# Kernel tuning notes

Hardware: AMD Instinct MI355X
Metric: run time of the kernel (lower is better)

Reference implementation:

```python
import jax, jax.numpy as jnp
import numpy as np

B, N, D = 8, 2048, 1024

def setup_inputs() -> dict:
    key = jax.random.key(0)
    ks = jax.random.split(key, 4)
    x = jax.random.normal(ks[0], (B, N, D), dtype=jnp.float32)
    # Glorot-uniform-like scaling as keras Dense default
    def glorot(k, shape):
        fan_in, fan_out = shape[0], shape[1]
        lim = jnp.sqrt(6.0 / (fan_in + fan_out)).astype(jnp.float32)
        return jax.random.uniform(k, shape, jnp.float32, -lim, lim)
    Wq = glorot(ks[1], (D, D))
    Wk = glorot(ks[2], (D, D))
    Wout = glorot(ks[3], (N, D))  # out_proj acts on last axis of [B,N,N] scores
    bq = jnp.zeros((D,), jnp.float32)
    bk = jnp.zeros((D,), jnp.float32)
    bout = jnp.zeros((D,), jnp.float32)
    return {"x": x, "Wq": Wq, "bq": bq, "Wk": Wk, "bk": bk, "Wout": Wout, "bout": bout}

def reference(x, Wq, bq, Wk, bk, Wout, bout):
    Q = x @ Wq + bq                                  # [B,N,D]
    K = x @ Wk + bk                                  # [B,N,D]
    scores = jnp.einsum("bnd,bmd->bnm", Q, K)       # [B,N,N] (no 1/sqrt(d) in source)
    A = jax.nn.softmax(scores, axis=-1)              # [B,N,N]
    return A @ Wout + bout                           # [B,N,D]
```

## Files before the change

### kernel.cpp

```cpp
#include <hip/hip_runtime.h>


typedef unsigned short u16;
typedef __bf16 bf16x8 __attribute__((ext_vector_type(8)));
typedef float f32x4 __attribute__((ext_vector_type(4)));

#define BB 8
#define NN 2048
#define DD 1024
#define MT (BB * NN)
#define PSTRIDE 4096

#define MFMA3(d, ah, al, bh, bl)                                         \
  d = __builtin_amdgcn_mfma_f32_16x16x32_bf16(ah, bh, d, 0, 0, 0);       \
  d = __builtin_amdgcn_mfma_f32_16x16x32_bf16(ah, bl, d, 0, 0, 0);       \
  d = __builtin_amdgcn_mfma_f32_16x16x32_bf16(al, bh, d, 0, 0, 0);

static __device__ __forceinline__ u16 f2bf(float f) {
  unsigned u = __builtin_bit_cast(unsigned, f);
  u += 0x7FFFu + ((u >> 16) & 1u);
  return (u16)(u >> 16);
}
static __device__ __forceinline__ float bf2f(u16 h) {
  unsigned u = ((unsigned)h) << 16;
  return __builtin_bit_cast(float, u);
}

static __device__ __forceinline__ void gload16(const void* g, void* l) {
  __builtin_amdgcn_global_load_lds((const __attribute__((address_space(1))) void*)g,
                                   (__attribute__((address_space(3))) void*)l, 16, 0, 0);
}

static __device__ __forceinline__ int swz_wg() {
  int nwg = gridDim.x;
  int orig = blockIdx.x;
  int q = nwg >> 3;
  return (orig & 7) * q + (orig >> 3);
}

#define SW(r) (((r) ^ ((r) >> 2)) & 3)

static __device__ __forceinline__ void stage_plane_sw(const u16* __restrict__ g0,
                                                      u16* lp0, int tid) {
#pragma unroll
  for (int j = 0; j < 2; j++) {
    int o = tid + j * 512;
    int row = o >> 2, c = o & 3;
    const u16* g = g0 + (size_t)row * DD + ((c ^ SW(row)) << 3);
    u16* lp = lp0 + (((tid >> 6) << 6) + j * 512) * 8;
    gload16(g, lp);
  }
}

static __device__ __forceinline__ bf16x8 rdfrag(const u16* plane, int row, int g4) {
  return *(const bf16x8*)&plane[row * 32 + ((g4 ^ SW(row)) << 3)];
}

template <bool STG, int VM>
static __device__ __forceinline__ void tile4(
    u16* Lc, const u16* Ah, const u16* Al, const u16* Bh, const u16* Bl, int kst,
    f32x4 (&acc)[8][4], int tid, int wm, int wn, int r16, int g4) {
  u16* PA0 = Lc;
  u16* PA1 = Lc + 8192;
  u16* PB0 = Lc + 16384;
  u16* PB1 = Lc + 24576;
  bf16x8 a0[4], a1[4], b0[4], b1[4];

#pragma unroll
  for (int fm = 0; fm < 4; fm++) {
    int rw = wm * 128 + fm * 16 + r16;
    a0[fm] = rdfrag(PA0, rw, g4);
    a1[fm] = rdfrag(PA1, rw, g4);
  }
#pragma unroll
  for (int fn = 0; fn < 2; fn++) {
    int rw = wn * 64 + fn * 16 + r16;
    b0[fn] = rdfrag(PB0, rw, g4);
    b1[fn] = rdfrag(PB1, rw, g4);
  }
  __builtin_amdgcn_s_barrier();
  asm volatile("s_waitcnt lgkmcnt(0)" ::: "memory");
  __builtin_amdgcn_s_setprio(1);
#pragma unroll
  for (int fm = 0; fm < 4; fm++)
#pragma unroll
    for (int fn = 0; fn < 2; fn++) { MFMA3(acc[fm][fn], a0[fm], a1[fm], b0[fn], b1[fn]); }
  __builtin_amdgcn_s_setprio(0);

#pragma unroll
  for (int fn = 2; fn < 4; fn++) {
    int rw = wn * 64 + fn * 16 + r16;
    b0[fn] = rdfrag(PB0, rw, g4);
    b1[fn] = rdfrag(PB1, rw, g4);
  }
  __builtin_amdgcn_s_barrier();
  asm volatile("s_waitcnt lgkmcnt(0)" ::: "memory");
  __builtin_amdgcn_s_setprio(1);
#pragma unroll
  for (int fm = 0; fm < 4; fm++)
#pragma unroll
    for (int fn = 2; fn < 4; fn++) { MFMA3(acc[fm][fn], a0[fm], a1[fm], b0[fn], b1[fn]); }
  __builtin_amdgcn_s_setprio(0);
  __builtin_amdgcn_s_barrier();

#pragma unroll
  for (int fm = 0; fm < 4; fm++) {
    int rw = wm * 128 + 64 + fm * 16 + r16;
    a0[fm] = rdfrag(PA0, rw, g4);
    a1[fm] = rdfrag(PA1, rw, g4);
  }
  if (STG) {
    stage_plane_sw(Bh + kst, PB0, tid);
    stage_plane_sw(Bl + kst, PB1, tid);
  }
  __builtin_amdgcn_s_barrier();
  asm volatile("s_waitcnt lgkmcnt(0)" ::: "memory");
  __builtin_amdgcn_s_setprio(1);
#pragma unroll
  for (int fm = 0; fm < 4; fm++)
#pragma unroll
    for (int fn = 0; fn < 2; fn++) { MFMA3(acc[fm + 4][fn], a0[fm], a1[fm], b0[fn], b1[fn]); }
  __builtin_amdgcn_s_setprio(0);
  __builtin_amdgcn_s_barrier();

  if (STG) {
    stage_plane_sw(Ah + kst, PA0, tid);
    stage_plane_sw(Al + kst, PA1, tid);
  }
  if (VM == 8) {
    asm volatile("s_waitcnt vmcnt(8)" ::: "memory");
  } else if (VM == 0) {
    asm volatile("s_waitcnt vmcnt(0)" ::: "memory");
  }
  __builtin_amdgcn_s_barrier();
  __builtin_amdgcn_s_setprio(1);
#pragma unroll
  for (int fm = 0; fm < 4; fm++)
#pragma unroll
    for (int fn = 2; fn < 4; fn++) { MFMA3(acc[fm + 4][fn], a0[fm], a1[fm], b0[fn], b1[fn]); }
  __builtin_amdgcn_s_setprio(0);
}

static __device__ __forceinline__ void mm8_core(u16* L, const u16* Ah, const u16* Al,
                                                const u16* Bh, const u16* Bl,
                                                f32x4 (&acc)[8][4], int tid) {
  int lane = tid & 63, r16 = lane & 15, g4 = lane >> 4;
  int w = tid >> 6, wm = w >> 2, wn = w & 3;
  u16* L0 = L;
  u16* L1 = L + 4 * 8192;
  stage_plane_sw(Ah + 0, L0 + 0, tid);
  stage_plane_sw(Al + 0, L0 + 8192, tid);
  stage_plane_sw(Bh + 0, L0 + 16384, tid);
  stage_plane_sw(Bl + 0, L0 + 24576, tid);
  stage_plane_sw(Ah + 32, L1 + 0, tid);
  stage_plane_sw(Al + 32, L1 + 8192, tid);
  stage_plane_sw(Bh + 32, L1 + 16384, tid);
  stage_plane_sw(Bl + 32, L1 + 24576, tid);
  asm volatile("s_waitcnt vmcnt(8)" ::: "memory");
  __builtin_amdgcn_s_barrier();
#pragma unroll 1
  for (int i = 0; i < 15; i++) {
    int t0 = 2 * i;
    tile4<true, 8>(L0, Ah, Al, Bh, Bl, (t0 + 2) * 32, acc, tid, wm, wn, r16, g4);
    tile4<true, 8>(L1, Ah, Al, Bh, Bl, (t0 + 3) * 32, acc, tid, wm, wn, r16, g4);
  }
  tile4<false, 0>(L0, Ah, Al, Bh, Bl, 0, acc, tid, wm, wn, r16, g4);
  tile4<false, -1>(L1, Ah, Al, Bh, Bl, 0, acc, tid, wm, wn, r16, g4);
}

__launch_bounds__(512, 2)
__global__ void k_gemm_s8(const u16* __restrict__ yh, const u16* __restrict__ yl,
                          const u16* __restrict__ xh, const u16* __restrict__ xl,
                          float* __restrict__ S) {
  __shared__ __attribute__((aligned(16))) u16 lds[2][4][8192];
  int wg = swz_wg();
  int nt = wg & 7, mtot = wg >> 3;
  int b = mtot >> 3, mt = mtot & 7;
  const size_t po = (size_t)b * NN * DD;
  const u16* Ah = yh + po + (size_t)(mt * 256) * DD;
  const u16* Al = yl + po + (size_t)(mt * 256) * DD;
  const u16* Bh = xh + po + (size_t)(nt * 256) * DD;
  const u16* Bl = xl + po + (size_t)(nt * 256) * DD;
  int tid = threadIdx.x;
  f32x4 acc[8][4] = {};
  mm8_core(&lds[0][0][0], Ah, Al, Bh, Bl, acc, tid);
  int lane = tid & 63, r16 = lane & 15, g4 = lane >> 4;
  int w = tid >> 6, wm = w >> 2, wn = w & 3;
  float* Sb = S + (size_t)b * NN * NN;
#pragma unroll
  for (int fm = 0; fm < 8; fm++)
#pragma unroll
    for (int fn = 0; fn < 4; fn++) {
      int col = nt * 256 + wn * 64 + fn * 16 + r16;
      int row = mt * 256 + wm * 128 + fm * 16 + g4 * 4;
#pragma unroll
      for (int i2 = 0; i2 < 4; i2++)
        Sb[(size_t)(row + i2) * NN + col] = acc[fm][fn][i2];
    }
}

__launch_bounds__(512, 2)
__global__ void k_gemm_y8(const u16* __restrict__ ah_g, const u16* __restrict__ al_g,
                          const u16* __restrict__ bh_g, const u16* __restrict__ bl_g,
                          u16* __restrict__ ohi, u16* __restrict__ olo) {
  __shared__ __attribute__((aligned(16))) u16 lds[2][4][8192];
  int wg = swz_wg();
  int nt = wg & 3, mt = wg >> 2;
  const u16* Ah = ah_g + (size_t)(mt * 256) * DD;
  const u16* Al = al_g + (size_t)(mt * 256) * DD;
  const u16* Bh = bh_g + (size_t)(nt * 256) * DD;
  const u16* Bl = bl_g + (size_t)(nt * 256) * DD;
  int tid = threadIdx.x;
  f32x4 acc[8][4] = {};
  mm8_core(&lds[0][0][0], Ah, Al, Bh, Bl, acc, tid);
  int lane = tid & 63, r16 = lane & 15, g4 = lane >> 4;
  int w = tid >> 6, wm = w >> 2, wn = w & 3;
#pragma unroll
  for (int fm = 0; fm < 8; fm++)
#pragma unroll
    for (int fn = 0; fn < 4; fn++) {
      int col = nt * 256 + wn * 64 + fn * 16 + r16;
      int row = mt * 256 + wm * 128 + fm * 16 + g4 * 4;
#pragma unroll
      for (int i2 = 0; i2 < 4; i2++) {
        float v = acc[fm][fn][i2];
        u16 h = f2bf(v);
        size_t o = (size_t)(row + i2) * DD + col;
        ohi[o] = h;
        olo[o] = f2bf(v - bf2f(h));
      }
    }
}

__global__ void k_split(const float* __restrict__ x, u16* __restrict__ hi,
                        u16* __restrict__ lo, long n4) {
  long i = (long)blockIdx.x * blockDim.x + threadIdx.x;
  long stride = (long)gridDim.x * blockDim.x;
  for (; i < n4; i += stride) {
    float4 v = ((const float4*)x)[i];
    u16 h0 = f2bf(v.x), h1 = f2bf(v.y), h2 = f2bf(v.z), h3 = f2bf(v.w);
    ushort4 hv; hv.x = h0; hv.y = h1; hv.z = h2; hv.w = h3;
    ushort4 lv;
    lv.x = f2bf(v.x - bf2f(h0)); lv.y = f2bf(v.y - bf2f(h1));
    lv.z = f2bf(v.z - bf2f(h2)); lv.w = f2bf(v.w - bf2f(h3));
    ((ushort4*)hi)[i] = hv;
    ((ushort4*)lo)[i] = lv;
  }
}

__global__ void k_transpose_split(const float* __restrict__ W, u16* __restrict__ thi,
                                  int R, int C) {
  __shared__ float tile[32][33];
  int c0 = blockIdx.x * 32, r0 = blockIdx.y * 32;
  int tx = threadIdx.x, ty = threadIdx.y;
#pragma unroll
  for (int i = 0; i < 4; i++)
    tile[ty + i * 8][tx] = W[(size_t)(r0 + ty + i * 8) * C + c0 + tx];
  __syncthreads();
#pragma unroll
  for (int i = 0; i < 4; i++) {
    float v = tile[tx][ty + i * 8];
    thi[(size_t)(c0 + ty + i * 8) * R + r0 + tx] = f2bf(v);
  }
}

__global__ void k_matvec(const float* __restrict__ A, const float* __restrict__ v,
                         float* __restrict__ out, int cols) {
  int w = threadIdx.x >> 6, lane = threadIdx.x & 63;
  int row = blockIdx.x * 4 + w;
  const float4* Ar = (const float4*)(A + (size_t)row * cols);
  const float4* vv = (const float4*)v;
  float s = 0.f;
  for (int j = lane; j < cols / 4; j += 64) {
    float4 a = Ar[j], b = vv[j];
    s += a.x * b.x + a.y * b.y + a.z * b.z + a.w * b.w;
  }
#pragma unroll
  for (int o = 32; o > 0; o >>= 1) s += __shfl_xor(s, o);
  if (lane == 0) out[row] = s;
}

__global__ void k_softmax(float* __restrict__ S, const float* __restrict__ c2, int nrows) {
  int w = threadIdx.x >> 6, lane = threadIdx.x & 63;
  int row = blockIdx.x * 4 + w;
  if (row >= nrows) return;
  const float4* Sr = (const float4*)(S + (size_t)row * NN);
  const float4* c2b = (const float4*)(c2 + ((size_t)(row >> 11) << 11));
  float4 v[8];
  float mx = -3.4e38f;
#pragma unroll
  for (int j = 0; j < 8; j++) {
    v[j] = Sr[j * 64 + lane];
    float4 c = c2b[j * 64 + lane];
    v[j].x += c.x; v[j].y += c.y; v[j].z += c.z; v[j].w += c.w;
    mx = fmaxf(mx, fmaxf(fmaxf(v[j].x, v[j].y), fmaxf(v[j].z, v[j].w)));
  }
#pragma unroll
  for (int o = 32; o > 0; o >>= 1) mx = fmaxf(mx, __shfl_xor(mx, o));
  float e[32];
  float sum = 0.f;
#pragma unroll
  for (int j = 0; j < 8; j++) {
    e[j * 4 + 0] = __expf(v[j].x - mx);
    e[j * 4 + 1] = __expf(v[j].y - mx);
    e[j * 4 + 2] = __expf(v[j].z - mx);
    e[j * 4 + 3] = __expf(v[j].w - mx);
    sum += e[j * 4 + 0] + e[j * 4 + 1] + e[j * 4 + 2] + e[j * 4 + 3];
  }
#pragma unroll
  for (int o = 32; o > 0; o >>= 1) sum += __shfl_xor(sum, o);
  float inv = 1.0f / sum;
  ushort4* Pr = (ushort4*)((u16*)S + (size_t)row * PSTRIDE);
#pragma unroll
  for (int j = 0; j < 8; j++) {
    ushort4 pv;
    pv.x = f2bf(e[j * 4 + 0] * inv);
    pv.y = f2bf(e[j * 4 + 1] * inv);
    pv.z = f2bf(e[j * 4 + 2] * inv);
    pv.w = f2bf(e[j * 4 + 3] * inv);
    Pr[j * 64 + lane] = pv;
  }
}

static __device__ __forceinline__ void stage_tile(const u16* __restrict__ gsrc,
                                                  u16* plane, int t, int ldg) {
  int w = t >> 6;
#pragma unroll
  for (int j = 0; j < 2; j++) {
    int idx = t + j * 256;
    const u16* g = gsrc + (size_t)(idx >> 2) * ldg + (idx & 3) * 8;
    u16* lp = plane + (w * 64 + j * 256) * 8;
    gload16(g, lp);
  }
}

__launch_bounds__(256)
__global__ void k_gemm_out(const u16* __restrict__ P, const u16* __restrict__ woutT,
                           const float* __restrict__ bout, float* __restrict__ out) {
  __shared__ __attribute__((aligned(16))) u16 lds[2][128][32];
  int wg = swz_wg();
  int b = wg >> 7, dt = wg & 7, ntt = (wg >> 3) & 15;
  const u16* Pb = P + (size_t)b * NN * PSTRIDE;
  float* ob = out + (size_t)b * NN * DD;

  int t = threadIdx.x, lane = t & 63, w = t >> 6;
  int wr = w >> 1, wc = w & 1, r16 = lane & 15, g = lane >> 4;

  f32x4 acc[4][4] = {};

  for (int k0 = 0; k0 < NN; k0 += 32) {
    stage_tile(Pb + (size_t)(ntt * 128) * PSTRIDE + k0, &lds[0][0][0], t, PSTRIDE);
    stage_tile(woutT + (size_t)(dt * 128) * NN + k0, &lds[1][0][0], t, NN);
    __syncthreads();
    bf16x8 bh[4];
#pragma unroll
    for (int fn = 0; fn < 4; fn++)
      bh[fn] = *(const bf16x8*)&lds[1][wc * 64 + fn * 16 + r16][g * 8];
#pragma unroll
    for (int fm = 0; fm < 4; fm++) {
      bf16x8 ah = *(const bf16x8*)&lds[0][wr * 64 + fm * 16 + r16][g * 8];
#pragma unroll
      for (int fn = 0; fn < 4; fn++)
        acc[fm][fn] = __builtin_amdgcn_mfma_f32_16x16x32_bf16(ah, bh[fn], acc[fm][fn], 0, 0, 0);
    }
    __syncthreads();
  }
#pragma unroll
  for (int fm = 0; fm < 4; fm++) {
#pragma unroll
    for (int fn = 0; fn < 4; fn++) {
      int col = dt * 128 + wc * 64 + fn * 16 + r16;
      float bv = bout[col];
      int row = ntt * 128 + wr * 64 + fm * 16 + g * 4;
#pragma unroll
      for (int i = 0; i < 4; i++)
        ob[(size_t)(row + i) * DD + col] = acc[fm][fn][i] + bv;
    }
  }
}

extern "C" void kernel_launch(void* const* d_in, const int* in_sizes, int n_in,
                              void* d_out, int out_size, void* d_ws, size_t ws_size,
                              hipStream_t stream) {
  const float* x = (const float*)d_in[0];
  const float* Wq = (const float*)d_in[1];
  const float* bq = (const float*)d_in[2];
  const float* Wk = (const float*)d_in[3];
  const float* bk = (const float*)d_in[4];
  const float* Wout = (const float*)d_in[5];
  const float* bout = (const float*)d_in[6];
  float* out = (float*)d_out;
  char* ws = (char*)d_ws;

  const size_t MB = 1ull << 20;
  u16* mth = (u16*)(ws + 0 * MB);
  u16* mtl = (u16*)(ws + 2 * MB);
  u16* woutT = (u16*)(ws + 4 * MB);
  float* v2 = (float*)(ws + 8 * MB);
  float* c2 = (float*)(ws + 8 * MB + 65536);
  char* base = ws + 12 * MB;

  dim3 tb(32, 8, 1);

  if (ws_size >= 204 * MB) {
    u16* xh = (u16*)(base);
    u16* xl = (u16*)(base + 32 * MB);
    u16* yh = (u16*)(base + 64 * MB);
    u16* yl = (u16*)(base + 96 * MB);
    char* R = base + 128 * MB;
    u16* wqh = (u16*)(R);
    u16* wql = (u16*)(R + 2 * MB);
    u16* wkh = (u16*)(R + 4 * MB);
    u16* wkl = (u16*)(R + 6 * MB);
    float* S = (float*)R;

    k_split<<<256, 256, 0, stream>>>(Wq, wqh, wql, (long)DD * DD / 4);
    k_split<<<256, 256, 0, stream>>>(Wk, wkh, wkl, (long)DD * DD / 4);
    k_gemm_y8<<<16, 512, 0, stream>>>(wkh, wkl, wqh, wql, mth, mtl);
    k_transpose_split<<<dim3(32, 64, 1), tb, 0, stream>>>(Wout, woutT, 2048, 1024);
    k_matvec<<<256, 256, 0, stream>>>(Wk, bq, v2, DD);
    k_matvec<<<4096, 256, 0, stream>>>(x, v2, c2, DD);
    k_split<<<2048, 256, 0, stream>>>(x, xh, xl, (long)MT * DD / 4);
    k_gemm_y8<<<256, 512, 0, stream>>>(xh, xl, mth, mtl, yh, yl);
    for (int h = 0; h < 2; h++) {
      size_t qo = (size_t)h * 4 * NN * DD;
      k_gemm_s8<<<256, 512, 0, stream>>>(yh + qo, yl + qo, xh + qo, xl + qo, S);
      k_softmax<<<4 * NN / 4, 256, 0, stream>>>(S, c2 + (size_t)h * 4 * NN, 4 * NN);
      k_gemm_out<<<4 * 128, 256, 0, stream>>>((const u16*)S, woutT, bout, out + qo);
    }
  } else if (ws_size >= 156 * MB) {
    u16* xh = (u16*)(base);
    u16* xl = (u16*)(base + 32 * MB);
    u16* yh = (u16*)(base + 64 * MB);
    u16* yl = (u16*)(base + 96 * MB);
    char* R = base + 128 * MB;
    u16* wqh = (u16*)(R);
    u16* wql = (u16*)(R + 2 * MB);
    u16* wkh = (u16*)(R + 4 * MB);
    u16* wkl = (u16*)(R + 6 * MB);
    float* S = (float*)R;

    k_split<<<256, 256, 0, stream>>>(Wq, wqh, wql, (long)DD * DD / 4);
    k_split<<<256, 256, 0, stream>>>(Wk, wkh, wkl, (long)DD * DD / 4);
    k_gemm_y8<<<16, 512, 0, stream>>>(wkh, wkl, wqh, wql, mth, mtl);
    k_transpose_split<<<dim3(32, 64, 1), tb, 0, stream>>>(Wout, woutT, 2048, 1024);
    k_matvec<<<256, 256, 0, stream>>>(Wk, bq, v2, DD);
    k_matvec<<<4096, 256, 0, stream>>>(x, v2, c2, DD);
    k_split<<<2048, 256, 0, stream>>>(x, xh, xl, (long)MT * DD / 4);
    k_gemm_y8<<<256, 512, 0, stream>>>(xh, xl, mth, mtl, yh, yl);
    for (int b = 0; b < BB; b++) {
      size_t qo = (size_t)b * NN * DD;
      k_gemm_s8<<<64, 512, 0, stream>>>(yh + qo, yl + qo, xh + qo, xl + qo, S);
      k_softmax<<<NN / 4, 256, 0, stream>>>(S, c2 + (size_t)b * NN, NN);
      k_gemm_out<<<128, 256, 0, stream>>>((const u16*)S, woutT, bout, out + qo);
    }
  } else {
    u16* xh = (u16*)(base);
    u16* xl = (u16*)(base + 8 * MB);
    u16* yh = (u16*)(base + 16 * MB);
    u16* yl = (u16*)(base + 24 * MB);
    char* R = base + 32 * MB;
    u16* wqh = (u16*)(R);
    u16* wql = (u16*)(R + 2 * MB);
    u16* wkh = (u16*)(R + 4 * MB);
    u16* wkl = (u16*)(R + 6 * MB);
    float* S = (float*)R;

    k_split<<<256, 256, 0, stream>>>(Wq, wqh, wql, (long)DD * DD / 4);
    k_split<<<256, 256, 0, stream>>>(Wk, wkh, wkl, (long)DD * DD / 4);
    k_gemm_y8<<<16, 512, 0, stream>>>(wkh, wkl, wqh, wql, mth, mtl);
    k_transpose_split<<<dim3(32, 64, 1), tb, 0, stream>>>(Wout, woutT, 2048, 1024);
    k_matvec<<<256, 256, 0, stream>>>(Wk, bq, v2, DD);
    k_matvec<<<4096, 256, 0, stream>>>(x, v2, c2, DD);
    for (int c = 0; c < 4; c++) {
      size_t xo = (size_t)c * 2 * NN * DD;
      k_split<<<1024, 256, 0, stream>>>(x + xo, xh, xl, (long)2 * NN * DD / 4);
      k_gemm_y8<<<64, 512, 0, stream>>>(xh, xl, mth, mtl, yh, yl);
      for (int bi = 0; bi < 2; bi++) {
        size_t lo = (size_t)bi * NN * DD;
        k_gemm_s8<<<64, 512, 0, stream>>>(yh + lo, yl + lo, xh + lo, xl + lo, S);
        k_softmax<<<NN / 4, 256, 0, stream>>>(S, c2 + (size_t)(c * 2 + bi) * NN, NN);
        k_gemm_out<<<128, 256, 0, stream>>>((const u16*)S, woutT, bout, out + xo + lo);
      }
    }
  }
}
```

Measured before the change: 522.7 us.

## Load A fragments directly from global into registers, stage only B in LDS

The GEMM core stops staging the A operand (hi/lo bf16 planes) through LDS. Each wave now reads its A fragments straight from global memory into registers, while B stays double-buffered in LDS. This halves LDS usage, removes several barriers per k-step and reorders the MFMA blocks. In exchange, A reads become uncoalesced 16-byte per-lane global loads, more vector registers are held, and the vmcnt wait depths change.

```diff
diff --git a/kernel.cpp b/kernel.cpp
--- a/kernel.cpp
+++ b/kernel.cpp
@@ -58,19 +58,16 @@
 
 template <bool STG, int VM>
 static __device__ __forceinline__ void tile4(
-    u16* Lc, const u16* Ah, const u16* Al, const u16* Bh, const u16* Bl, int kst,
-    f32x4 (&acc)[8][4], int tid, int wm, int wn, int r16, int g4) {
-  u16* PA0 = Lc;
-  u16* PA1 = Lc + 8192;
-  u16* PB0 = Lc + 16384;
-  u16* PB1 = Lc + 24576;
-  bf16x8 a0[4], a1[4], b0[4], b1[4];
-
-#pragma unroll
-  for (int fm = 0; fm < 4; fm++) {
-    int rw = wm * 128 + fm * 16 + r16;
-    a0[fm] = rdfrag(PA0, rw, g4);
-    a1[fm] = rdfrag(PA1, rw, g4);
+    u16* Lc, const u16* aPH, const u16* aPL, const u16* Bh, const u16* Bl,
+    int k0, int kst, f32x4 (&acc)[8][4], int tid, int wn, int r16, int g4) {
+  u16* PB0 = Lc;
+  u16* PB1 = Lc + 8192;
+  bf16x8 aH[8], aL[8], b0[4], b1[4];
+
+#pragma unroll
+  for (int fm = 0; fm < 8; fm++) {
+    aH[fm] = *(const bf16x8*)(aPH + (size_t)fm * 16 * DD + k0);
+    aL[fm] = *(const bf16x8*)(aPL + (size_t)fm * 16 * DD + k0);
   }
 #pragma unroll
   for (int fn = 0; fn < 2; fn++) {
@@ -78,13 +75,11 @@
     b0[fn] = rdfrag(PB0, rw, g4);
     b1[fn] = rdfrag(PB1, rw, g4);
   }
-  __builtin_amdgcn_s_barrier();
-  asm volatile("s_waitcnt lgkmcnt(0)" ::: "memory");
   __builtin_amdgcn_s_setprio(1);
 #pragma unroll
   for (int fm = 0; fm < 4; fm++)
 #pragma unroll
-    for (int fn = 0; fn < 2; fn++) { MFMA3(acc[fm][fn], a0[fm], a1[fm], b0[fn], b1[fn]); }
+    for (int fn = 0; fn < 2; fn++) { MFMA3(acc[fm][fn], aH[fm], aL[fm], b0[fn], b1[fn]); }
   __builtin_amdgcn_s_setprio(0);
 
 #pragma unroll
@@ -93,51 +88,39 @@
     b0[fn] = rdfrag(PB0, rw, g4);
     b1[fn] = rdfrag(PB1, rw, g4);
   }
+  __builtin_amdgcn_s_setprio(1);
+#pragma unroll
+  for (int fm = 4; fm < 8; fm++)
+#pragma unroll
+    for (int fn = 0; fn < 2; fn++) { MFMA3(acc[fm][fn], aH[fm], aL[fm], b0[fn], b1[fn]); }
+  __builtin_amdgcn_s_setprio(0);
+  asm volatile("s_waitcnt lgkmcnt(0)" ::: "memory");
   __builtin_amdgcn_s_barrier();
-  asm volatile("s_waitcnt lgkmcnt(0)" ::: "memory");
-  __builtin_amdgcn_s_setprio(1);
-#pragma unroll
-  for (int fm = 0; fm < 4; fm++)
-#pragma unroll
-    for (int fn = 2; fn < 4; fn++) { MFMA3(acc[fm][fn], a0[fm], a1[fm], b0[fn], b1[fn]); }
-  __builtin_amdgcn_s_setprio(0);
-  __builtin_amdgcn_s_barrier();
-
-#pragma unroll
-  for (int fm = 0; fm < 4; fm++) {
-    int rw = wm * 128 + 64 + fm * 16 + r16;
-    a0[fm] = rdfrag(PA0, rw, g4);
-    a1[fm] = rdfrag(PA1, rw, g4);
-  }
+
   if (STG) {
     stage_plane_sw(Bh + kst, PB0, tid);
     stage_plane_sw(Bl + kst, PB1, tid);
   }
-  __builtin_amdgcn_s_barrier();
-  asm volatile("s_waitcnt lgkmcnt(0)" ::: "memory");
   __builtin_amdgcn_s_setprio(1);
 #pragma unroll
   for (int fm = 0; fm < 4; fm++)
 #pragma unroll
-    for (int fn = 0; fn < 2; fn++) { MFMA3(acc[fm + 4][fn], a0[fm], a1[fm], b0[fn], b1[fn]); }
+    for (int fn = 2; fn < 4; fn++) { MFMA3(acc[fm][fn], aH[fm], aL[fm], b0[fn], b1[fn]); }
   __builtin_amdgcn_s_setprio(0);
-  __builtin_amdgcn_s_barrier();
-
-  if (STG) {
-    stage_plane_sw(Ah + kst, PA0, tid);
-    stage_plane_sw(Al + kst, PA1, tid);
-  }
-  if (VM == 8) {
-    asm volatile("s_waitcnt vmcnt(8)" ::: "memory");
+
+  if (VM == 20) {
+    asm volatile("s_waitcnt vmcnt(20)" ::: "memory");
+  } else if (VM == 16) {
+    asm volatile("s_waitcnt vmcnt(16)" ::: "memory");
   } else if (VM == 0) {
     asm volatile("s_waitcnt vmcnt(0)" ::: "memory");
   }
   __builtin_amdgcn_s_barrier();
   __builtin_amdgcn_s_setprio(1);
 #pragma unroll
-  for (int fm = 0; fm < 4; fm++)
-#pragma unroll
-    for (int fn = 2; fn < 4; fn++) { MFMA3(acc[fm + 4][fn], a0[fm], a1[fm], b0[fn], b1[fn]); }
+  for (int fm = 4; fm < 8; fm++)
+#pragma unroll
+    for (int fn = 2; fn < 4; fn++) { MFMA3(acc[fm][fn], aH[fm], aL[fm], b0[fn], b1[fn]); }
   __builtin_amdgcn_s_setprio(0);
 }
 
@@ -147,32 +130,30 @@
   int lane = tid & 63, r16 = lane & 15, g4 = lane >> 4;
   int w = tid >> 6, wm = w >> 2, wn = w & 3;
   u16* L0 = L;
-  u16* L1 = L + 4 * 8192;
-  stage_plane_sw(Ah + 0, L0 + 0, tid);
-  stage_plane_sw(Al + 0, L0 + 8192, tid);
-  stage_plane_sw(Bh + 0, L0 + 16384, tid);
-  stage_plane_sw(Bl + 0, L0 + 24576, tid);
-  stage_plane_sw(Ah + 32, L1 + 0, tid);
-  stage_plane_sw(Al + 32, L1 + 8192, tid);
-  stage_plane_sw(Bh + 32, L1 + 16384, tid);
-  stage_plane_sw(Bl + 32, L1 + 24576, tid);
-  asm volatile("s_waitcnt vmcnt(8)" ::: "memory");
+  u16* L1 = L + 16384;
+  const u16* aPH = Ah + (size_t)(wm * 128 + r16) * DD + g4 * 8;
+  const u16* aPL = Al + (size_t)(wm * 128 + r16) * DD + g4 * 8;
+  stage_plane_sw(Bh + 0, L0, tid);
+  stage_plane_sw(Bl + 0, L0 + 8192, tid);
+  stage_plane_sw(Bh + 32, L1, tid);
+  stage_plane_sw(Bl + 32, L1 + 8192, tid);
+  asm volatile("s_waitcnt vmcnt(4)" ::: "memory");
   __builtin_amdgcn_s_barrier();
 #pragma unroll 1
   for (int i = 0; i < 15; i++) {
     int t0 = 2 * i;
-    tile4<true, 8>(L0, Ah, Al, Bh, Bl, (t0 + 2) * 32, acc, tid, wm, wn, r16, g4);
-    tile4<true, 8>(L1, Ah, Al, Bh, Bl, (t0 + 3) * 32, acc, tid, wm, wn, r16, g4);
-  }
-  tile4<false, 0>(L0, Ah, Al, Bh, Bl, 0, acc, tid, wm, wn, r16, g4);
-  tile4<false, -1>(L1, Ah, Al, Bh, Bl, 0, acc, tid, wm, wn, r16, g4);
+    tile4<true, 20>(L0, aPH, aPL, Bh, Bl, t0 * 32, (t0 + 2) * 32, acc, tid, wn, r16, g4);
+    tile4<true, 20>(L1, aPH, aPL, Bh, Bl, (t0 + 1) * 32, (t0 + 3) * 32, acc, tid, wn, r16, g4);
+  }
+  tile4<false, 16>(L0, aPH, aPL, Bh, Bl, 30 * 32, 0, acc, tid, wn, r16, g4);
+  tile4<false, -1>(L1, aPH, aPL, Bh, Bl, 31 * 32, 0, acc, tid, wn, r16, g4);
 }
 
 __launch_bounds__(512, 2)
 __global__ void k_gemm_s8(const u16* __restrict__ yh, const u16* __restrict__ yl,
                           const u16* __restrict__ xh, const u16* __restrict__ xl,
                           float* __restrict__ S) {
-  __shared__ __attribute__((aligned(16))) u16 lds[2][4][8192];
+  __shared__ __attribute__((aligned(16))) u16 lds[2][2][8192];
   int wg = swz_wg();
   int nt = wg & 7, mtot = wg >> 3;
   int b = mtot >> 3, mt = mtot & 7;
@@ -203,7 +184,7 @@
 __global__ void k_gemm_y8(const u16* __restrict__ ah_g, const u16* __restrict__ al_g,
                           const u16* __restrict__ bh_g, const u16* __restrict__ bl_g,
                           u16* __restrict__ ohi, u16* __restrict__ olo) {
-  __shared__ __attribute__((aligned(16))) u16 lds[2][4][8192];
+  __shared__ __attribute__((aligned(16))) u16 lds[2][2][8192];
   int wg = swz_wg();
   int nt = wg & 3, mt = wg >> 2;
   const u16* Ah = ah_g + (size_t)(mt * 256) * DD;
```

New measurement: 992.0 us. 1.9x slower.

## Rewrite output GEMM as pipelined 256x256 tile kernel and fuse x split with matvec

Applied to the files above, without the earlier changes.

Replaces the simple 128x128 output GEMM, which synchronised twice per K step, with a 512-thread 256x256-tile kernel. The new kernel uses swizzled double-buffered LDS, asynchronous global-to-LDS loads and interleaved MFMA phases, matching the score GEMM's pipeline. It also fuses the x·v2 matvec into the x hi/lo split kernel so x is read once instead of twice. Fewer, larger workgroups (128 or 32 per launch) may underfill the GPU's compute units, especially on the per-batch paths.

```diff
diff --git a/kernel.cpp b/kernel.cpp
--- a/kernel.cpp
+++ b/kernel.cpp
@@ -41,12 +41,12 @@
 #define SW(r) (((r) ^ ((r) >> 2)) & 3)
 
 static __device__ __forceinline__ void stage_plane_sw(const u16* __restrict__ g0,
-                                                      u16* lp0, int tid) {
+                                                      u16* lp0, int tid, int ld) {
 #pragma unroll
   for (int j = 0; j < 2; j++) {
     int o = tid + j * 512;
     int row = o >> 2, c = o & 3;
-    const u16* g = g0 + (size_t)row * DD + ((c ^ SW(row)) << 3);
+    const u16* g = g0 + (size_t)row * ld + ((c ^ SW(row)) << 3);
     u16* lp = lp0 + (((tid >> 6) << 6) + j * 512) * 8;
     gload16(g, lp);
   }
@@ -110,8 +110,8 @@
     a1[fm] = rdfrag(PA1, rw, g4);
   }
   if (STG) {
-    stage_plane_sw(Bh + kst, PB0, tid);
-    stage_plane_sw(Bl + kst, PB1, tid);
+    stage_plane_sw(Bh + kst, PB0, tid, DD);
+    stage_plane_sw(Bl + kst, PB1, tid, DD);
   }
   __builtin_amdgcn_s_barrier();
   asm volatile("s_waitcnt lgkmcnt(0)" ::: "memory");
@@ -124,8 +124,8 @@
   __builtin_amdgcn_s_barrier();
 
   if (STG) {
-    stage_plane_sw(Ah + kst, PA0, tid);
-    stage_plane_sw(Al + kst, PA1, tid);
+    stage_plane_sw(Ah + kst, PA0, tid, DD);
+    stage_plane_sw(Al + kst, PA1, tid, DD);
   }
   if (VM == 8) {
     asm volatile("s_waitcnt vmcnt(8)" ::: "memory");
@@ -148,14 +148,14 @@
   int w = tid >> 6, wm = w >> 2, wn = w & 3;
   u16* L0 = L;
   u16* L1 = L + 4 * 8192;
-  stage_plane_sw(Ah + 0, L0 + 0, tid);
-  stage_plane_sw(Al + 0, L0 + 8192, tid);
-  stage_plane_sw(Bh + 0, L0 + 16384, tid);
-  stage_plane_sw(Bl + 0, L0 + 24576, tid);
-  stage_plane_sw(Ah + 32, L1 + 0, tid);
-  stage_plane_sw(Al + 32, L1 + 8192, tid);
-  stage_plane_sw(Bh + 32, L1 + 16384, tid);
-  stage_plane_sw(Bl + 32, L1 + 24576, tid);
+  stage_plane_sw(Ah + 0, L0 + 0, tid, DD);
+  stage_plane_sw(Al + 0, L0 + 8192, tid, DD);
+  stage_plane_sw(Bh + 0, L0 + 16384, tid, DD);
+  stage_plane_sw(Bl + 0, L0 + 24576, tid, DD);
+  stage_plane_sw(Ah + 32, L1 + 0, tid, DD);
+  stage_plane_sw(Al + 32, L1 + 8192, tid, DD);
+  stage_plane_sw(Bh + 32, L1 + 16384, tid, DD);
+  stage_plane_sw(Bl + 32, L1 + 24576, tid, DD);
   asm volatile("s_waitcnt vmcnt(8)" ::: "memory");
   __builtin_amdgcn_s_barrier();
 #pragma unroll 1
@@ -232,6 +232,116 @@
     }
 }
 
+template <bool STG, int VM>
+static __device__ __forceinline__ void tile4p(
+    u16* Lc, const u16* Ag, const u16* Bg, int kst, int ldA,
+    f32x4 (&acc)[8][4], int tid, int wm, int wn, int r16, int g4) {
+  u16* PA = Lc;
+  u16* PB = Lc + 8192;
+  bf16x8 a0[4], b4[4];
+
+#pragma unroll
+  for (int fm = 0; fm < 4; fm++) a0[fm] = rdfrag(PA, wm * 128 + fm * 16 + r16, g4);
+#pragma unroll
+  for (int fn = 0; fn < 2; fn++) b4[fn] = rdfrag(PB, wn * 64 + fn * 16 + r16, g4);
+  __builtin_amdgcn_s_barrier();
+  asm volatile("s_waitcnt lgkmcnt(0)" ::: "memory");
+  __builtin_amdgcn_s_setprio(1);
+#pragma unroll
+  for (int fm = 0; fm < 4; fm++)
+#pragma unroll
+    for (int fn = 0; fn < 2; fn++)
+      acc[fm][fn] = __builtin_amdgcn_mfma_f32_16x16x32_bf16(a0[fm], b4[fn], acc[fm][fn], 0, 0, 0);
+  __builtin_amdgcn_s_setprio(0);
+
+#pragma unroll
+  for (int fn = 2; fn < 4; fn++) b4[fn] = rdfrag(PB, wn * 64 + fn * 16 + r16, g4);
+  __builtin_amdgcn_s_barrier();
+  asm volatile("s_waitcnt lgkmcnt(0)" ::: "memory");
+  __builtin_amdgcn_s_setprio(1);
+#pragma unroll
+  for (int fm = 0; fm < 4; fm++)
+#pragma unroll
+    for (int fn = 2; fn < 4; fn++)
+      acc[fm][fn] = __builtin_amdgcn_mfma_f32_16x16x32_bf16(a0[fm], b4[fn], acc[fm][fn], 0, 0, 0);
+  __builtin_amdgcn_s_setprio(0);
+  __builtin_amdgcn_s_barrier();
+
+#pragma unroll
+  for (int fm = 0; fm < 4; fm++) a0[fm] = rdfrag(PA, wm * 128 + 64 + fm * 16 + r16, g4);
+  if (STG) stage_plane_sw(Bg + kst, PB, tid, NN);
+  __builtin_amdgcn_s_barrier();
+  asm volatile("s_waitcnt lgkmcnt(0)" ::: "memory");
+  __builtin_amdgcn_s_setprio(1);
+#pragma unroll
+  for (int fm = 0; fm < 4; fm++)
+#pragma unroll
+    for (int fn = 0; fn < 2; fn++)
+      acc[fm + 4][fn] = __builtin_amdgcn_mfma_f32_16x16x32_bf16(a0[fm], b4[fn], acc[fm + 4][fn], 0, 0, 0);
+  __builtin_amdgcn_s_setprio(0);
+  __builtin_amdgcn_s_barrier();
+
+  if (STG) stage_plane_sw(Ag + kst, PA, tid, ldA);
+  if (VM == 4) {
+    asm volatile("s_waitcnt vmcnt(4)" ::: "memory");
+  } else if (VM == 0) {
+    asm volatile("s_waitcnt vmcnt(0)" ::: "memory");
+  }
+  __builtin_amdgcn_s_barrier();
+  __builtin_amdgcn_s_setprio(1);
+#pragma unroll
+  for (int fm = 0; fm < 4; fm++)
+#pragma unroll
+    for (int fn = 2; fn < 4; fn++)
+      acc[fm + 4][fn] = __builtin_amdgcn_mfma_f32_16x16x32_bf16(a0[fm], b4[fn], acc[fm + 4][fn], 0, 0, 0);
+  __builtin_amdgcn_s_setprio(0);
+}
+
+__launch_bounds__(512, 2)
+__global__ void k_gemm_out(const u16* __restrict__ P, const u16* __restrict__ woutT,
+                           const float* __restrict__ bout, float* __restrict__ out) {
+  __shared__ __attribute__((aligned(16))) u16 lds[2][2][8192];
+  int wg = swz_wg();
+  int b = wg >> 5, mt = (wg >> 2) & 7, nt = wg & 3;
+  const u16* Ag = P + (size_t)b * NN * PSTRIDE + (size_t)(mt * 256) * PSTRIDE;
+  const u16* Bg = woutT + (size_t)(nt * 256) * NN;
+  float* ob = out + (size_t)b * NN * DD;
+
+  int tid = threadIdx.x;
+  int lane = tid & 63, r16 = lane & 15, g4 = lane >> 4;
+  int w = tid >> 6, wm = w >> 2, wn = w & 3;
+  u16* L0 = &lds[0][0][0];
+  u16* L1 = &lds[1][0][0];
+
+  f32x4 acc[8][4] = {};
+  stage_plane_sw(Ag + 0, L0, tid, PSTRIDE);
+  stage_plane_sw(Bg + 0, L0 + 8192, tid, NN);
+  stage_plane_sw(Ag + 32, L1, tid, PSTRIDE);
+  stage_plane_sw(Bg + 32, L1 + 8192, tid, NN);
+  asm volatile("s_waitcnt vmcnt(4)" ::: "memory");
+  __builtin_amdgcn_s_barrier();
+#pragma unroll 1
+  for (int i = 0; i < 31; i++) {
+    int t0 = 2 * i;
+    tile4p<true, 4>(L0, Ag, Bg, (t0 + 2) * 32, PSTRIDE, acc, tid, wm, wn, r16, g4);
+    tile4p<true, 4>(L1, Ag, Bg, (t0 + 3) * 32, PSTRIDE, acc, tid, wm, wn, r16, g4);
+  }
+  tile4p<false, 0>(L0, Ag, Bg, 0, PSTRIDE, acc, tid, wm, wn, r16, g4);
+  tile4p<false, -1>(L1, Ag, Bg, 0, PSTRIDE, acc, tid, wm, wn, r16, g4);
+
+#pragma unroll
+  for (int fm = 0; fm < 8; fm++)
+#pragma unroll
+    for (int fn = 0; fn < 4; fn++) {
+      int col = nt * 256 + wn * 64 + fn * 16 + r16;
+      float bv = bout[col];
+      int row = mt * 256 + wm * 128 + fm * 16 + g4 * 4;
+#pragma unroll
+      for (int i2 = 0; i2 < 4; i2++)
+        ob[(size_t)(row + i2) * DD + col] = acc[fm][fn][i2] + bv;
+    }
+}
+
 __global__ void k_split(const float* __restrict__ x, u16* __restrict__ hi,
                         u16* __restrict__ lo, long n4) {
   long i = (long)blockIdx.x * blockDim.x + threadIdx.x;
@@ -248,6 +358,35 @@
   }
 }
 
+__global__ void k_split_x(const float* __restrict__ x, const float* __restrict__ v2,
+                          u16* __restrict__ hi, u16* __restrict__ lo,
+                          float* __restrict__ c2) {
+  int w = threadIdx.x >> 6, lane = threadIdx.x & 63;
+  int row = blockIdx.x * 4 + w;
+  const float4* xr = (const float4*)(x + (size_t)row * DD);
+  const float4* vv = (const float4*)v2;
+  ushort4* hr = (ushort4*)(hi + (size_t)row * DD);
+  ushort4* lr = (ushort4*)(lo + (size_t)row * DD);
+  float s = 0.f;
+#pragma unroll
+  for (int j = 0; j < 4; j++) {
+    int idx = j * 64 + lane;
+    float4 v = xr[idx];
+    float4 b = vv[idx];
+    s += v.x * b.x + v.y * b.y + v.z * b.z + v.w * b.w;
+    u16 h0 = f2bf(v.x), h1 = f2bf(v.y), h2 = f2bf(v.z), h3 = f2bf(v.w);
+    ushort4 hv; hv.x = h0; hv.y = h1; hv.z = h2; hv.w = h3;
+    ushort4 lv;
+    lv.x = f2bf(v.x - bf2f(h0)); lv.y = f2bf(v.y - bf2f(h1));
+    lv.z = f2bf(v.z - bf2f(h2)); lv.w = f2bf(v.w - bf2f(h3));
+    hr[idx] = hv;
+    lr[idx] = lv;
+  }
+#pragma unroll
+  for (int o = 32; o > 0; o >>= 1) s += __shfl_xor(s, o);
+  if (lane == 0) c2[row] = s;
+}
+
 __global__ void k_transpose_split(const float* __restrict__ W, u16* __restrict__ thi,
                                   int R, int C) {
   __shared__ float tile[32][33];
@@ -319,63 +458,6 @@
     pv.z = f2bf(e[j * 4 + 2] * inv);
     pv.w = f2bf(e[j * 4 + 3] * inv);
     Pr[j * 64 + lane] = pv;
-  }
-}
-
-static __device__ __forceinline__ void stage_tile(const u16* __restrict__ gsrc,
-                                                  u16* plane, int t, int ldg) {
-  int w = t >> 6;
-#pragma unroll
-  for (int j = 0; j < 2; j++) {
-    int idx = t + j * 256;
-    const u16* g = gsrc + (size_t)(idx >> 2) * ldg + (idx & 3) * 8;
-    u16* lp = plane + (w * 64 + j * 256) * 8;
-    gload16(g, lp);
-  }
-}
-
-__launch_bounds__(256)
-__global__ void k_gemm_out(const u16* __restrict__ P, const u16* __restrict__ woutT,
-                           const float* __restrict__ bout, float* __restrict__ out) {
-  __shared__ __attribute__((aligned(16))) u16 lds[2][128][32];
-  int wg = swz_wg();
-  int b = wg >> 7, dt = wg & 7, ntt = (wg >> 3) & 15;
-  const u16* Pb = P + (size_t)b * NN * PSTRIDE;
-  float* ob = out + (size_t)b * NN * DD;
-
-  int t = threadIdx.x, lane = t & 63, w = t >> 6;
-  int wr = w >> 1, wc = w & 1, r16 = lane & 15, g = lane >> 4;
-
-  f32x4 acc[4][4] = {};
-
-  for (int k0 = 0; k0 < NN; k0 += 32) {
-    stage_tile(Pb + (size_t)(ntt * 128) * PSTRIDE + k0, &lds[0][0][0], t, PSTRIDE);
-    stage_tile(woutT + (size_t)(dt * 128) * NN + k0, &lds[1][0][0], t, NN);
-    __syncthreads();
-    bf16x8 bh[4];
-#pragma unroll
-    for (int fn = 0; fn < 4; fn++)
-      bh[fn] = *(const bf16x8*)&lds[1][wc * 64 + fn * 16 + r16][g * 8];
-#pragma unroll
-    for (int fm = 0; fm < 4; fm++) {
-      bf16x8 ah = *(const bf16x8*)&lds[0][wr * 64 + fm * 16 + r16][g * 8];
-#pragma unroll
-      for (int fn = 0; fn < 4; fn++)
-        acc[fm][fn] = __builtin_amdgcn_mfma_f32_16x16x32_bf16(ah, bh[fn], acc[fm][fn], 0, 0, 0);
-    }
-    __syncthreads();
-  }
-#pragma unroll
-  for (int fm = 0; fm < 4; fm++) {
-#pragma unroll
-    for (int fn = 0; fn < 4; fn++) {
-      int col = dt * 128 + wc * 64 + fn * 16 + r16;
-      float bv = bout[col];
-      int row = ntt * 128 + wr * 64 + fm * 16 + g * 4;
-#pragma unroll
-      for (int i = 0; i < 4; i++)
-        ob[(size_t)(row + i) * DD + col] = acc[fm][fn][i] + bv;
-    }
   }
 }
 
@@ -419,14 +501,13 @@
     k_gemm_y8<<<16, 512, 0, stream>>>(wkh, wkl, wqh, wql, mth, mtl);
     k_transpose_split<<<dim3(32, 64, 1), tb, 0, stream>>>(Wout, woutT, 2048, 1024);
     k_matvec<<<256, 256, 0, stream>>>(Wk, bq, v2, DD);
-    k_matvec<<<4096, 256, 0, stream>>>(x, v2, c2, DD);
-    k_split<<<2048, 256, 0, stream>>>(x, xh, xl, (long)MT * DD / 4);
+    k_split_x<<<MT / 4, 256, 0, stream>>>(x, v2, xh, xl, c2);
     k_gemm_y8<<<256, 512, 0, stream>>>(xh, xl, mth, mtl, yh, yl);
     for (int h = 0; h < 2; h++) {
       size_t qo = (size_t)h * 4 * NN * DD;
       k_gemm_s8<<<256, 512, 0, stream>>>(yh + qo, yl + qo, xh + qo, xl + qo, S);
       k_softmax<<<4 * NN / 4, 256, 0, stream>>>(S, c2 + (size_t)h * 4 * NN, 4 * NN);
-      k_gemm_out<<<4 * 128, 256, 0, stream>>>((const u16*)S, woutT, bout, out + qo);
+      k_gemm_out<<<4 * 32, 512, 0, stream>>>((const u16*)S, woutT, bout, out + qo);
     }
   } else if (ws_size >= 156 * MB) {
     u16* xh = (u16*)(base);
@@ -445,14 +526,13 @@
     k_gemm_y8<<<16, 512, 0, stream>>>(wkh, wkl, wqh, wql, mth, mtl);
     k_transpose_split<<<dim3(32, 64, 1), tb, 0, stream>>>(Wout, woutT, 2048, 1024);
     k_matvec<<<256, 256, 0, stream>>>(Wk, bq, v2, DD);
-    k_matvec<<<4096, 256, 0, stream>>>(x, v2, c2, DD);
-    k_split<<<2048, 256, 0, stream>>>(x, xh, xl, (long)MT * DD / 4);
+    k_split_x<<<MT / 4, 256, 0, stream>>>(x, v2, xh, xl, c2);
     k_gemm_y8<<<256, 512, 0, stream>>>(xh, xl, mth, mtl, yh, yl);
     for (int b = 0; b < BB; b++) {
       size_t qo = (size_t)b * NN * DD;
       k_gemm_s8<<<64, 512, 0, stream>>>(yh + qo, yl + qo, xh + qo, xl + qo, S);
       k_softmax<<<NN / 4, 256, 0, stream>>>(S, c2 + (size_t)b * NN, NN);
-      k_gemm_out<<<128, 256, 0, stream>>>((const u16*)S, woutT, bout, out + qo);
+      k_gemm_out<<<32, 512, 0, stream>>>((const u16*)S, woutT, bout, out + qo);
     }
   } else {
     u16* xh = (u16*)(base);
@@ -471,16 +551,15 @@
     k_gemm_y8<<<16, 512, 0, stream>>>(wkh, wkl, wqh, wql, mth, mtl);
     k_transpose_split<<<dim3(32, 64, 1), tb, 0, stream>>>(Wout, woutT, 2048, 1024);
     k_matvec<<<256, 256, 0, stream>>>(Wk, bq, v2, DD);
-    k_matvec<<<4096, 256, 0, stream>>>(x, v2, c2, DD);
     for (int c = 0; c < 4; c++) {
       size_t xo = (size_t)c * 2 * NN * DD;
-      k_split<<<1024, 256, 0, stream>>>(x + xo, xh, xl, (long)2 * NN * DD / 4);
+      k_split_x<<<2 * NN / 4, 256, 0, stream>>>(x + xo, v2, xh, xl, c2 + (size_t)c * 2 * NN);
       k_gemm_y8<<<64, 512, 0, stream>>>(xh, xl, mth, mtl, yh, yl);
       for (int bi = 0; bi < 2; bi++) {
         size_t lo = (size_t)bi * NN * DD;
         k_gemm_s8<<<64, 512, 0, stream>>>(yh + lo, yl + lo, xh + lo, xl + lo, S);
         k_softmax<<<NN / 4, 256, 0, stream>>>(S, c2 + (size_t)(c * 2 + bi) * NN, NN);
-        k_gemm_out<<<128, 256, 0, stream>>>((const u16*)S, woutT, bout, out + xo + lo);
+        k_gemm_out<<<32, 512, 0, stream>>>((const u16*)S, woutT, bout, out + xo + lo);
       }
     }
   }
```

Result: no change. 512.6 us (-1.9%).
